# Kernel tuning notes

Hardware: AMD Instinct MI355X
Metric: run time of the kernel (lower is better)

Reference implementation:

```python
import jax, jax.numpy as jnp
import numpy as np

B, C, V = 65536, 2, 3          # batch of coords, coord_dim, value_dim
D, K, S = 64, 1024, 4          # latent_dim, num_codes, num_latent_vectors (VQ stages)
H, L, F = 1024, 5, 25          # hidden_size, num_layers, num_freqs
IN = C * (2 * F + 1)           # 102: positional-encoded decoder input
COMMIT = 0.25


def setup_inputs() -> dict:
    key = jax.random.key(0)
    ks = jax.random.split(key, 12)
    coords = jax.random.uniform(ks[0], (B, C), jnp.float32, -1.0, 1.0)
    latents = jax.random.normal(ks[1], (1, S, D), jnp.float32)
    cb = jax.random.normal(ks[2], (S, K, D), jnp.float32)
    codebooks = cb / jnp.linalg.norm(cb, axis=-1, keepdims=True)  # unit-norm init as in module
    mod_W = jax.random.normal(ks[3], (L, D, H), jnp.float32) / np.sqrt(D)
    mod_b = jax.random.normal(ks[4], (L, H), jnp.float32) * 0.01
    dec_W0 = jax.random.normal(ks[5], (IN, H), jnp.float32) / np.sqrt(IN)
    dec_b0 = jax.random.normal(ks[6], (H,), jnp.float32) * 0.01
    dec_Wh = jax.random.normal(ks[7], (L - 1, H, H), jnp.float32) / np.sqrt(H)
    dec_bh = jax.random.normal(ks[8], (L - 1, H), jnp.float32) * 0.01
    dec_Wout = jax.random.normal(ks[9], (H, V), jnp.float32) / np.sqrt(H)
    dec_bout = jax.random.normal(ks[10], (V,), jnp.float32) * 0.01
    return dict(coords=coords, latent_idx=0, latents=latents, codebooks=codebooks,
                mod_W=mod_W, mod_b=mod_b, dec_W0=dec_W0, dec_b0=dec_b0,
                dec_Wh=dec_Wh, dec_bh=dec_bh, dec_Wout=dec_Wout, dec_bout=dec_bout)


def _vq(z, emb):
    # z: (1, D), emb: (K, D) -> squared-distance argmin + straight-through
    d = jnp.sum(z * z, axis=1, keepdims=True) - 2.0 * (z @ emb.T) + jnp.sum(emb * emb, axis=1)
    idx = jnp.argmin(d, axis=1)               # (1,)
    z_q = emb[idx]                            # (1, D)
    z_q_st = z_q + jax.lax.stop_gradient(z - z_q)   # fwd value == z, grad flows to embedding
    loss = COMMIT * jnp.mean((jax.lax.stop_gradient(z_q) - z) ** 2)
    return z_q_st, idx, loss


def reference(coords, latent_idx, latents, codebooks, mod_W, mod_b,
              dec_W0, dec_b0, dec_Wh, dec_bh, dec_Wout, dec_bout):
    img = latents[latent_idx]                 # (S, D)
    z_q_sum = jnp.zeros((1, D), coords.dtype)
    residual_target = jnp.zeros((1, D), coords.dtype)
    total_vq_loss = 0.0
    idxs = []
    for s in range(S):                        # residual VQ over fixed small #stages
        z_stage = img[s:s + 1]
        if s == 0:
            residual_target = z_stage
            z_cur = z_stage
        else:
            residual_target = residual_target + z_stage
            z_cur = residual_target - jax.lax.stop_gradient(z_q_sum)
        z_q_st, idx, l = _vq(z_cur, codebooks[s])
        z_q_sum = z_q_sum + z_q_st
        total_vq_loss = total_vq_loss + l
        idxs.append(idx)
    # modulation betas from the (same-for-all-rows) quantized latent; broadcast over B
    betas = jnp.einsum('od,ldh->loh', z_q_sum, mod_W) + mod_b[:, None, :]   # (L, 1, H)
    # positional encoding: [x, sin(pi*f0*x), cos(pi*f0*x), sin(pi*f1*x), ...]
    freqs = 2.0 ** jnp.arange(F, dtype=coords.dtype)
    ang = coords[:, None, :] * (freqs[None, :, None] * jnp.pi)              # (B, F, C)
    pe = jnp.concatenate(
        [coords, jnp.stack([jnp.sin(ang), jnp.cos(ang)], axis=2).reshape(coords.shape[0], -1)],
        axis=-1)                                                            # (B, IN)
    h = jax.nn.relu(pe @ dec_W0 + dec_b0 + betas[0])
    for i in range(L - 1):
        h = jax.nn.relu(h @ dec_Wh[i] + dec_bh[i] + betas[i + 1])
    values = h @ dec_Wout + dec_bout                                        # (B, V)
    return values, jnp.stack(idxs), total_vq_loss
```

## Files before the change

kernel.cpp:

```cpp
#include <hip/hip_runtime.h>
#include <hip/hip_bf16.h>
#include <stdint.h>

#define NB   65536
#define NC   2
#define NV   3
#define ND   64
#define NK   1024
#define NS   4
#define NH   1024
#define NL   5
#define NF   25
#define NIN  102
#define K0P  128

typedef float f32x4 __attribute__((ext_vector_type(4)));
typedef int   i32x4 __attribute__((ext_vector_type(4)));
typedef int   i32x8 __attribute__((ext_vector_type(8)));
typedef unsigned char u8;

__device__ __forceinline__ u8 to_fp8(float x) {
    return (u8)(__builtin_amdgcn_cvt_pk_fp8_f32(x, 0.0f, 0, false) & 0xff);
}


__global__ __launch_bounds__(1024) void vq_kernel(
    const float* __restrict__ latents, const int* __restrict__ latent_idx,
    const float* __restrict__ codebooks, float* __restrict__ zq_out,
    float* __restrict__ out) {
    __shared__ float zcur[ND], resid[ND], zqsum[ND], ssq[ND];
    __shared__ float sDw[16];
    __shared__ int   sKw[16];
    __shared__ int   sBest;
    int t = threadIdx.x, lane = t & 63, wv = t >> 6;
    const float* img = latents + (size_t)latent_idx[0] * (NS * ND);
    if (t < ND) { resid[t] = 0.f; zqsum[t] = 0.f; }
    __syncthreads();
    float lossAcc = 0.f;
    for (int s = 0; s < NS; s++) {
        if (t < ND) {
            float iv = img[s * ND + t];
            float r  = resid[t] + iv;
            resid[t] = r;
            zcur[t]  = (s == 0) ? iv : (r - zqsum[t]);
        }
        __syncthreads();
        float zz = 0.f;
#pragma unroll
        for (int d = 0; d < ND; d++) { float z = zcur[d]; zz += z * z; }
        const float4* e4 = (const float4*)(codebooks + ((size_t)s * NK + t) * ND);
        float dot = 0.f, ee = 0.f;
#pragma unroll
        for (int i = 0; i < 16; i++) {
            float4 v = e4[i];
            dot += zcur[4 * i + 0] * v.x; dot += zcur[4 * i + 1] * v.y;
            dot += zcur[4 * i + 2] * v.z; dot += zcur[4 * i + 3] * v.w;
            ee  += v.x * v.x; ee += v.y * v.y; ee += v.z * v.z; ee += v.w * v.w;
        }
        float dmin = zz - 2.0f * dot + ee;
        int   kmin = t;
#pragma unroll
        for (int m = 1; m < 64; m <<= 1) {
            float d2 = __shfl_xor(dmin, m);
            int   k2 = __shfl_xor(kmin, m);
            if (d2 < dmin || (d2 == dmin && k2 < kmin)) { dmin = d2; kmin = k2; }
        }
        if (lane == 0) { sDw[wv] = dmin; sKw[wv] = kmin; }
        __syncthreads();
        if (t == 0) {
            float bd = sDw[0]; int bk = sKw[0];
            for (int w = 1; w < 16; w++) {
                float d2 = sDw[w]; int k2 = sKw[w];
                if (d2 < bd || (d2 == bd && k2 < bk)) { bd = d2; bk = k2; }
            }
            sBest = bk;
            out[NB * NV + s] = (float)bk;
        }
        __syncthreads();
        int best = sBest;
        const float* eb = codebooks + ((size_t)s * NK + best) * ND;
        if (t < ND) {
            float zq = eb[t];
            float d  = zq - zcur[t];
            ssq[t]   = d * d;
            zqsum[t] = zqsum[t] + (zq + (zcur[t] - zq));
        }
        __syncthreads();
        if (t == 0) {
            float sum = 0.f;
            for (int d = 0; d < ND; d++) sum += ssq[d];
            lossAcc += 0.25f * (sum / (float)ND);
        }
    }
    if (t < ND) zq_out[t] = zqsum[t];
    if (t == 0) out[NB * NV + NS] = lossAcc;
}

__global__ __launch_bounds__(256) void betas_kernel(
    const float* __restrict__ zq, const float* __restrict__ mod_W,
    const float* __restrict__ mod_b, const float* __restrict__ b0,
    const float* __restrict__ bh, float* __restrict__ bb) {
    int g = blockIdx.x * 256 + threadIdx.x;
    int l = g >> 10, n = g & 1023;
    float acc = mod_b[g];
    for (int d = 0; d < ND; d++) acc += zq[d] * mod_W[(size_t)(l * ND + d) * NH + n];
    acc += (l == 0) ? b0[n] : bh[(size_t)(l - 1) * NH + n];
    bb[g] = acc;
}

__global__ __launch_bounds__(256) void init_out_kernel(
    const float* __restrict__ bout, float* __restrict__ out) {
    int g = blockIdx.x * 256 + threadIdx.x;
    out[g] = bout[g % NV];
}

__global__ __launch_bounds__(256) void prep_kernel(
    const float* __restrict__ src, u8* __restrict__ dst, int Ks, int Kp) {
    __shared__ float tile[32][33];
    int nIt = Kp >> 7;
    src += (size_t)blockIdx.z * Ks * NH;
    dst += (size_t)blockIdx.z * NH * Kp;
    int k0 = blockIdx.x * 32, n0 = blockIdx.y * 32;
    int tx = threadIdx.x, ty = threadIdx.y;
    for (int i = 0; i < 4; i++) {
        int k = k0 + ty + i * 8;
        int n = n0 + tx;
        tile[ty + i * 8][tx] = (k < Ks) ? src[(size_t)k * NH + n] : 0.0f;
    }
    __syncthreads();
    int it = k0 >> 7, q = (k0 >> 5) & 3;
    for (int i = 0; i < 4; i++) {
        int n = n0 + ty + i * 8;
        int k = k0 + tx;
        int bn = n >> 7, j = (n >> 4) & 7, r16 = n & 15;
        size_t flat = ((size_t)(((bn * nIt + it) * 8 + j) * 64 + q * 16 + r16)) * 32 + tx;
        dst[flat] = to_fp8(tile[tx][ty + i * 8] * 64.0f);
    }
}

__device__ __forceinline__ float pe_val(const float* coords, int m, int k) {
    if (k < 2) return coords[m * 2 + k];
    if (k >= NIN) return 0.0f;
    int u = k - 2;
    int f = u >> 2, r = u & 3;
    float c = coords[m * 2 + (r & 1)];
    float a = c * __builtin_ldexpf(3.14159274101257324f, f);
    return (r < 2) ? sinf(a) : cosf(a);
}

__global__ __launch_bounds__(256) void pe_kernel(
    const float* __restrict__ coords, u8* __restrict__ pe) {
    int g = blockIdx.x * 256 + threadIdx.x;
    int m = g >> 5, k4 = (g & 31) * 4;
    float v0 = pe_val(coords, m, k4 + 0);
    float v1 = pe_val(coords, m, k4 + 1);
    float v2 = pe_val(coords, m, k4 + 2);
    float v3 = pe_val(coords, m, k4 + 3);
    int p = __builtin_amdgcn_cvt_pk_fp8_f32(v0, v1, 0, false);
    p     = __builtin_amdgcn_cvt_pk_fp8_f32(v2, v3, p, true);
    int m16 = m >> 4, r = m & 15, c32 = k4 >> 5, b = k4 & 31;
    *(int*)(pe + ((size_t)(m16 * 4 + c32) * 16 + r) * 32 + b) = p;
}

template <int MODE, int KT>
__global__ __launch_bounds__(256, 2) void gemm_kernel(
    const u8* __restrict__ A, const u8* __restrict__ W,
    const float* __restrict__ bb, u8* __restrict__ O,
    const float* __restrict__ Wout, float* __restrict__ out, int Mb) {
    __shared__ __align__(16) u8 smem[32768];
    int t   = threadIdx.x;
    int fid = blockIdx.x;
    int xcd = fid & 7;
    int j8  = fid >> 3;
    int bn  = j8 & 7;
    int bm  = xcd * (Mb >> 3) + (j8 >> 3);
    int lane = t & 63, wm = t >> 6;
    int q    = lane >> 4, r16 = lane & 15;
    const int nIt = KT >> 7;

    const u8* wbase = W + (size_t)(bn * nIt) * 16384 + lane * 32;
    const u8* abase = A + ((size_t)(bm * 16 + wm * 4) * (KT >> 5)) * 512 + lane * 32;

    f32x4 acc[4][8];
    f32x4 zero = {0.f, 0.f, 0.f, 0.f};
    for (int i = 0; i < 4; i++)
        for (int j = 0; j < 8; j++) acc[i][j] = zero;

#pragma unroll 2
    for (int it = 0; it < nIt; it++) {
        i32x8 bfr[8];
#pragma unroll
        for (int j = 0; j < 8; j++) {
            const u8* p = wbase + (size_t)(it * 8 + j) * 2048;
            i32x4 lo = *(const i32x4*)(p);
            i32x4 hi = *(const i32x4*)(p + 16);
            bfr[j] = __builtin_shufflevector(lo, hi, 0, 1, 2, 3, 4, 5, 6, 7);
        }
#pragma unroll
        for (int i = 0; i < 4; i++) {
            const u8* p = abase + ((size_t)i * (KT >> 5) + it * 4) * 512;
            i32x4 lo = *(const i32x4*)(p);
            i32x4 hi = *(const i32x4*)(p + 16);
            i32x8 af = __builtin_shufflevector(lo, hi, 0, 1, 2, 3, 4, 5, 6, 7);
#pragma unroll
            for (int j = 0; j < 8; j++)
                acc[i][j] = __builtin_amdgcn_mfma_scale_f32_16x16x128_f8f6f4(
                    bfr[j], af, acc[i][j], 0, 0,
                    0, 0x79797979,
                    0, 0x7f7f7f7f);
        }
    }

    if constexpr (MODE == 0) {
        u8* eb = smem;
#pragma unroll
        for (int i = 0; i < 4; i++) {
#pragma unroll
            for (int j = 0; j < 8; j++) {
                int nl = j * 16 + q * 4;
                f32x4 b4 = *(const f32x4*)(bb + bn * 128 + nl);
                float v0 = fmaxf(acc[i][j][0] + b4[0], 0.0f);
                float v1 = fmaxf(acc[i][j][1] + b4[1], 0.0f);
                float v2 = fmaxf(acc[i][j][2] + b4[2], 0.0f);
                float v3 = fmaxf(acc[i][j][3] + b4[3], 0.0f);
                int p = __builtin_amdgcn_cvt_pk_fp8_f32(v0, v1, 0, false);
                p     = __builtin_amdgcn_cvt_pk_fp8_f32(v2, v3, p, true);
                int idx = (((wm * 4 + i) * 4 + (j >> 1)) * 16 + r16) * 32
                        + (j & 1) * 16 + q * 4;
                *(int*)(eb + idx) = p;
            }
        }
        __syncthreads();
#pragma unroll
        for (int rd = 0; rd < 8; rd++) {
            int g2  = rd * 256 + t;
            int seg = g2 >> 5, off = (g2 & 31) * 16;
            int m16l = seg >> 2, c32l = seg & 3;
            i32x4 v = *(const i32x4*)(eb + seg * 512 + off);
            *(i32x4*)(O + ((size_t)((bm * 16 + m16l) * 32 + bn * 4 + c32l)) * 512 + off) = v;
        }
    } else {
#pragma unroll
        for (int i = 0; i < 4; i++) {
            float p0 = 0.f, p1 = 0.f, p2 = 0.f;
#pragma unroll
            for (int j = 0; j < 8; j++) {
                int nb = bn * 128 + j * 16 + q * 4;
                f32x4 b4 = *(const f32x4*)(bb + nb);
#pragma unroll
                for (int r = 0; r < 4; r++) {
                    float val = fmaxf(acc[i][j][r] + b4[r], 0.0f);
                    const float* w = Wout + (size_t)(nb + r) * NV;
                    p0 += val * w[0]; p1 += val * w[1]; p2 += val * w[2];
                }
            }
            p0 += __shfl_xor(p0, 16); p0 += __shfl_xor(p0, 32);
            p1 += __shfl_xor(p1, 16); p1 += __shfl_xor(p1, 32);
            p2 += __shfl_xor(p2, 16); p2 += __shfl_xor(p2, 32);
            if (q == 0) {
                int m = bm * 256 + wm * 64 + i * 16 + r16;
                atomicAdd(&out[(size_t)m * NV + 0], p0);
                atomicAdd(&out[(size_t)m * NV + 1], p1);
                atomicAdd(&out[(size_t)m * NV + 2], p2);
            }
        }
    }
}

extern "C" void kernel_launch(void* const* d_in, const int* in_sizes, int n_in,
                              void* d_out, int out_size, void* d_ws, size_t ws_size,
                              hipStream_t stream) {
    const float* coords     = (const float*)d_in[0];
    const int*   latent_idx = (const int*)d_in[1];
    const float* latents    = (const float*)d_in[2];
    const float* codebooks  = (const float*)d_in[3];
    const float* mod_W      = (const float*)d_in[4];
    const float* mod_b      = (const float*)d_in[5];
    const float* dec_W0     = (const float*)d_in[6];
    const float* dec_b0     = (const float*)d_in[7];
    const float* dec_Wh     = (const float*)d_in[8];
    const float* dec_bh     = (const float*)d_in[9];
    const float* dec_Wout   = (const float*)d_in[10];
    const float* dec_bout   = (const float*)d_in[11];
    float* out = (float*)d_out;

    char* wsb = (char*)d_ws;
    float* zq  = (float*)(wsb + 0);
    float* bb  = (float*)(wsb + 256);
    u8*    W0T = (u8*)(wsb + 20736);
    u8*    WhT = (u8*)(wsb + 151808);
    const size_t fixed_end = 4346368;

    int Bc = 65536;
    while (Bc > 2048 && fixed_end + 2 * (size_t)Bc * NH > ws_size)
        Bc >>= 1;
    int Mb = Bc / 256;

    u8* hA = (u8*)(wsb + fixed_end);
    u8* hB = hA + (size_t)Bc * NH;
    u8* pe = hB;

    vq_kernel<<<1, 1024, 0, stream>>>(latents, latent_idx, codebooks, zq, out);
    betas_kernel<<<20, 256, 0, stream>>>(zq, mod_W, mod_b, dec_b0, dec_bh, bb);
    init_out_kernel<<<(NB * NV) / 256, 256, 0, stream>>>(dec_bout, out);
    prep_kernel<<<dim3(4, 32, 1), dim3(32, 8), 0, stream>>>(dec_W0, W0T, NIN, K0P);
    prep_kernel<<<dim3(32, 32, 4), dim3(32, 8), 0, stream>>>(dec_Wh, WhT, NH, NH);

    for (int c0 = 0; c0 < NB; c0 += Bc) {
        pe_kernel<<<(Bc * 32) / 256, 256, 0, stream>>>(coords + (size_t)c0 * NC, pe);
        gemm_kernel<0, K0P><<<8 * Mb, 256, 0, stream>>>(
            pe, W0T, bb + 0 * NH, hA, nullptr, nullptr, Mb);
        gemm_kernel<0, NH><<<8 * Mb, 256, 0, stream>>>(
            hA, WhT + 0 * (size_t)NH * NH, bb + 1 * NH, hB, nullptr, nullptr, Mb);
        gemm_kernel<0, NH><<<8 * Mb, 256, 0, stream>>>(
            hB, WhT + 1 * (size_t)NH * NH, bb + 2 * NH, hA, nullptr, nullptr, Mb);
        gemm_kernel<0, NH><<<8 * Mb, 256, 0, stream>>>(
            hA, WhT + 2 * (size_t)NH * NH, bb + 3 * NH, hB, nullptr, nullptr, Mb);
        gemm_kernel<1, NH><<<8 * Mb, 256, 0, stream>>>(
            hB, WhT + 3 * (size_t)NH * NH, bb + 4 * NH, nullptr,
            dec_Wout, out + (size_t)c0 * NV, Mb);
    }
}
```

Baseline: 511.7 us.

## Stage weight tiles in LDS via async global_load_lds with double buffering

Result: faster. 473.7 us (-7.4%).

```diff
diff --git a/kernel.cpp b/kernel.cpp
--- a/kernel.cpp
+++ b/kernel.cpp
@@ -18,6 +18,13 @@
 typedef int   i32x4 __attribute__((ext_vector_type(4)));
 typedef int   i32x8 __attribute__((ext_vector_type(8)));
 typedef unsigned char u8;
+
+__device__ __forceinline__ void load_lds16(const void* g, void* l) {
+    __builtin_amdgcn_global_load_lds(
+        (const __attribute__((address_space(1))) void*)g,
+        (__attribute__((address_space(3))) void*)l,
+        16, 0, 0);
+}
 
 __device__ __forceinline__ u8 to_fp8(float x) {
     return (u8)(__builtin_amdgcn_cvt_pk_fp8_f32(x, 0.0f, 0, false) & 0xff);
@@ -128,12 +135,13 @@
         tile[ty + i * 8][tx] = (k < Ks) ? src[(size_t)k * NH + n] : 0.0f;
     }
     __syncthreads();
-    int it = k0 >> 7, q = (k0 >> 5) & 3;
     for (int i = 0; i < 4; i++) {
         int n = n0 + ty + i * 8;
         int k = k0 + tx;
         int bn = n >> 7, j = (n >> 4) & 7, r16 = n & 15;
-        size_t flat = ((size_t)(((bn * nIt + it) * 8 + j) * 64 + q * 16 + r16)) * 32 + tx;
+        int it = k >> 7, q = (k >> 5) & 3, half = (k >> 4) & 1, b16 = k & 15;
+        size_t flat = ((size_t)(((bn * nIt + it) * 8 + j) * 2 + half)) * 1024
+                    + (q * 16 + r16) * 16 + b16;
         dst[flat] = to_fp8(tile[tx][ty + i * 8] * 64.0f);
     }
 }
@@ -168,6 +176,8 @@
     const float* __restrict__ bb, u8* __restrict__ O,
     const float* __restrict__ Wout, float* __restrict__ out, int Mb) {
     __shared__ __align__(16) u8 smem[32768];
+    u8* sW0 = smem;
+    u8* sW1 = smem + 16384;
     int t   = threadIdx.x;
     int fid = blockIdx.x;
     int xcd = fid & 7;
@@ -178,7 +188,7 @@
     int q    = lane >> 4, r16 = lane & 15;
     const int nIt = KT >> 7;
 
-    const u8* wbase = W + (size_t)(bn * nIt) * 16384 + lane * 32;
+    const u8* wslab = W + (size_t)(bn * nIt) * 16384;
     const u8* abase = A + ((size_t)(bm * 16 + wm * 4) * (KT >> 5)) * 512 + lane * 32;
 
     f32x4 acc[4][8];
@@ -186,29 +196,55 @@
     for (int i = 0; i < 4; i++)
         for (int j = 0; j < 8; j++) acc[i][j] = zero;
 
-#pragma unroll 2
+#pragma unroll
+    for (int p = 0; p < 4; p++) {
+        int g = p * 256 + t;
+        load_lds16((const void*)(wslab + g * 16), (void*)(sW0 + g * 16));
+    }
+    i32x8 afc[4], afn[4];
+#pragma unroll
+    for (int i = 0; i < 4; i++) {
+        const u8* p = abase + ((size_t)i * (KT >> 5)) * 512;
+        i32x4 lo = *(const i32x4*)(p);
+        i32x4 hi = *(const i32x4*)(p + 16);
+        afc[i] = __builtin_shufflevector(lo, hi, 0, 1, 2, 3, 4, 5, 6, 7);
+    }
+    __syncthreads();
+
+#pragma unroll 1
     for (int it = 0; it < nIt; it++) {
-        i32x8 bfr[8];
+        u8* bufc = (it & 1) ? sW1 : sW0;
+        u8* bufn = (it & 1) ? sW0 : sW1;
+        if (it + 1 < nIt) {
+            const u8* ws = wslab + (size_t)(it + 1) * 16384;
+#pragma unroll
+            for (int p = 0; p < 4; p++) {
+                int g = p * 256 + t;
+                load_lds16((const void*)(ws + g * 16), (void*)(bufn + g * 16));
+            }
+#pragma unroll
+            for (int i = 0; i < 4; i++) {
+                const u8* p = abase + ((size_t)i * (KT >> 5) + (it + 1) * 4) * 512;
+                i32x4 lo = *(const i32x4*)(p);
+                i32x4 hi = *(const i32x4*)(p + 16);
+                afn[i] = __builtin_shufflevector(lo, hi, 0, 1, 2, 3, 4, 5, 6, 7);
+            }
+        }
 #pragma unroll
         for (int j = 0; j < 8; j++) {
-            const u8* p = wbase + (size_t)(it * 8 + j) * 2048;
-            i32x4 lo = *(const i32x4*)(p);
-            i32x4 hi = *(const i32x4*)(p + 16);
-            bfr[j] = __builtin_shufflevector(lo, hi, 0, 1, 2, 3, 4, 5, 6, 7);
-        }
-#pragma unroll
-        for (int i = 0; i < 4; i++) {
-            const u8* p = abase + ((size_t)i * (KT >> 5) + it * 4) * 512;
-            i32x4 lo = *(const i32x4*)(p);
-            i32x4 hi = *(const i32x4*)(p + 16);
-            i32x8 af = __builtin_shufflevector(lo, hi, 0, 1, 2, 3, 4, 5, 6, 7);
-#pragma unroll
-            for (int j = 0; j < 8; j++)
+            i32x4 lo = *(const i32x4*)(bufc + j * 2048 + lane * 16);
+            i32x4 hi = *(const i32x4*)(bufc + j * 2048 + 1024 + lane * 16);
+            i32x8 bfr = __builtin_shufflevector(lo, hi, 0, 1, 2, 3, 4, 5, 6, 7);
+#pragma unroll
+            for (int i = 0; i < 4; i++)
                 acc[i][j] = __builtin_amdgcn_mfma_scale_f32_16x16x128_f8f6f4(
-                    bfr[j], af, acc[i][j], 0, 0,
+                    bfr, afc[i], acc[i][j], 0, 0,
                     0, 0x79797979,
                     0, 0x7f7f7f7f);
         }
+        __syncthreads();
+#pragma unroll
+        for (int i = 0; i < 4; i++) afc[i] = afn[i];
     }
 
     if constexpr (MODE == 0) {
```
